# Kernel tuning notes

Hardware: AMD Instinct MI355X
Metric: run time of the kernel (lower is better)

## Reference

```python
import jax, jax.numpy as jnp
import numpy as np


def setup_inputs() -> dict:
    key = jax.random.key(0)
    k1, k2, k3, k4 = jax.random.split(key, 4)
    B, S, D = 16, 1024, 300      # batch, set_size, word_vector_dim
    K = 64                        # hidden_set_size == compressed_dim (element_dim)
    O = 256                       # set_representation_dim (output_dim)
    Xs = jax.random.normal(k1, (B, S, D), dtype=jnp.float32)
    # Linear(word_vector_dim -> hidden_set_size)
    W = jax.random.normal(k2, (K, D), dtype=jnp.float32) * (1.0 / np.sqrt(D))
    b = jax.random.normal(k3, (K,), dtype=jnp.float32) * 0.01
    # hidden_sets: (output_dim, hidden_set_size, element_dim) with xavier-normal scale
    xav = np.sqrt(2.0 / (K + K))
    hidden_sets = jax.random.normal(k4, (O, K, K), dtype=jnp.float32) * xav
    return {"Xs": Xs, "W": W, "b": b, "hidden_sets": hidden_sets}


def reference(Xs, W, b, hidden_sets):
    # compress: [B,S,D] @ [D,K] + b -> [B,S,K]
    Xc = jnp.einsum('bsd,kd->bsk', Xs, W) + b
    # bipartite_match: tensordot over element_dim -> [B,S,O,N] (N = hidden_set_size)
    G = jax.nn.relu(jnp.einsum('bsk,onk->bson', Xc, hidden_sets))
    # set_size (1024) > hidden_set_size (64): max over hidden-set axis, sum over set axis
    value = jnp.sum(jnp.max(G, axis=-1), axis=1)  # [B,O]
    return value
```

## Files before the change

kernel.cpp:

```cpp
#include <hip/hip_runtime.h>
#include <hip/hip_bf16.h>

#define B_  16
#define S_  1024
#define D_  300
#define DP  320
#define K_  64
#define O_  256
#define M_  (B_*S_)

#define LROW 80

typedef __attribute__((ext_vector_type(8)))  short s8b;
typedef __attribute__((ext_vector_type(4)))  float f32x4;
typedef __attribute__((ext_vector_type(16))) float f32x16;

#define MFMA16(a,b,c) __builtin_amdgcn_mfma_f32_16x16x32_bf16((a),(b),(c),0,0,0)
#define MFMA32(a,b,c) __builtin_amdgcn_mfma_f32_32x32x16_bf16((a),(b),(c),0,0,0)

__device__ __forceinline__ unsigned short bf16_bits(float f) {
    return __builtin_bit_cast(unsigned short, __float2bfloat16(f));
}

#define H_BLK  512
#define W_BLK  10
__global__ __launch_bounds__(256) void k_convert(
        const float* __restrict__ W, const float* __restrict__ H,
        __hip_bfloat16* __restrict__ Wb, __hip_bfloat16* __restrict__ Hb,
        float* __restrict__ out) {
    int bx = blockIdx.x, t = threadIdx.x;
    if (bx < H_BLK) {
        int g = (bx * 256 + t) * 8;
        float4 f0 = *(const float4*)(H + g);
        float4 f1 = *(const float4*)(H + g + 4);
        union { unsigned short us[8]; uint4 q; } pk;
        pk.us[0]=bf16_bits(f0.x); pk.us[1]=bf16_bits(f0.y);
        pk.us[2]=bf16_bits(f0.z); pk.us[3]=bf16_bits(f0.w);
        pk.us[4]=bf16_bits(f1.x); pk.us[5]=bf16_bits(f1.y);
        pk.us[6]=bf16_bits(f1.z); pk.us[7]=bf16_bits(f1.w);
        *(uint4*)(Hb + g) = pk.q;
        return;
    }
    if (bx == H_BLK + W_BLK) {
        float4 z = {0.f,0.f,0.f,0.f};
        float4* o4 = (float4*)out;
#pragma unroll
        for (int i = 0; i < 4; ++i) o4[t * 4 + i] = z;
        return;
    }
    int g = (bx - H_BLK) * 256 + t;
    int r = g / 40, c = (g - r * 40) * 8;
    const float* src = W + (size_t)r * D_;
    float v[8];
    if (c + 8 <= D_) {
        float4 f0 = *(const float4*)(src + c);
        float4 f1 = *(const float4*)(src + c + 4);
        v[0]=f0.x; v[1]=f0.y; v[2]=f0.z; v[3]=f0.w;
        v[4]=f1.x; v[5]=f1.y; v[6]=f1.z; v[7]=f1.w;
    } else {
#pragma unroll
        for (int j = 0; j < 8; ++j) v[j] = (c + j < D_) ? src[c + j] : 0.0f;
    }
    union { unsigned short us[8]; uint4 q; } pk;
#pragma unroll
    for (int j = 0; j < 8; ++j) pk.us[j] = bf16_bits(v[j]);
    *(uint4*)(Wb + (size_t)r * DP + c) = pk.q;
}

__global__ __launch_bounds__(256) void k_compress(
        const float* __restrict__ Xs,
        const __hip_bfloat16* __restrict__ Wb,
        const float* __restrict__ bias,
        __hip_bfloat16* __restrict__ Xc) {
    int tid  = threadIdx.x;
    int w    = tid >> 6, lane = tid & 63;
    int q    = lane >> 4, r = lane & 15;
    int row0 = blockIdx.x * 16;
    int col0 = w * 16;

    f32x4 acc0 = {0.f,0.f,0.f,0.f}, acc1 = {0.f,0.f,0.f,0.f};
    const float*          arow = Xs + (size_t)(row0 + r) * D_;
    const __hip_bfloat16* brow = Wb + (size_t)(col0 + r) * DP;
    const float4 z4 = {0.f,0.f,0.f,0.f};

#pragma unroll
    for (int ks = 0; ks < 10; ++ks) {
        int k0 = ks * 32 + q * 8;
        float4 f0 = (k0     < D_) ? *(const float4*)(arow + k0)     : z4;
        float4 f1 = (k0 + 4 < D_) ? *(const float4*)(arow + k0 + 4) : z4;
        union { unsigned short us[8]; s8b v; } pk;
        pk.us[0]=bf16_bits(f0.x); pk.us[1]=bf16_bits(f0.y);
        pk.us[2]=bf16_bits(f0.z); pk.us[3]=bf16_bits(f0.w);
        pk.us[4]=bf16_bits(f1.x); pk.us[5]=bf16_bits(f1.y);
        pk.us[6]=bf16_bits(f1.z); pk.us[7]=bf16_bits(f1.w);
        s8b b = __builtin_bit_cast(s8b, *(const uint4*)(brow + k0));
        if (ks & 1) acc1 = MFMA16(pk.v, b, acc1);
        else        acc0 = MFMA16(pk.v, b, acc0);
    }
#pragma unroll
    for (int i = 0; i < 4; ++i) {
        int orow = row0 + q * 4 + i;
        int c    = col0 + r;
        Xc[(size_t)orow * K_ + c] =
            __float2bfloat16(acc0[i] + acc1[i] + bias[c]);
    }
}

__global__ __launch_bounds__(256, 4) void k_fused(
        const __hip_bfloat16* __restrict__ Xc,
        const __hip_bfloat16* __restrict__ Hb,
        float* __restrict__ out) {
    __shared__ __hip_bfloat16 lx[2][64 * LROW];
    int tid   = threadIdx.x;
    int w     = tid >> 6, lane = tid & 63;
    int half  = lane >> 5, l31 = lane & 31;
    int bx    = blockIdx.x;
    int batch = bx >> 7;
    int oq    = (bx >> 1) & 63;
    int sh    = bx & 1;
    int o     = oq * 4 + w;

    s8b af[2][4];
#pragma unroll
    for (int nt = 0; nt < 2; ++nt) {
        const __hip_bfloat16* hrow =
            Hb + (size_t)(o * 64 + nt * 32 + l31) * 64 + half * 8;
#pragma unroll
        for (int ks = 0; ks < 4; ++ks)
            af[nt][ks] = __builtin_bit_cast(s8b, *(const uint4*)(hrow + ks * 16));
    }

    const __hip_bfloat16* xbase =
        Xc + ((size_t)batch * S_ + (size_t)sh * 512) * K_;

    int sr = tid >> 3, sc = tid & 7;

#pragma unroll
    for (int i = 0; i < 2; ++i) {
        int r = sr + i * 32;
        uint4 v = *(const uint4*)(xbase + (size_t)r * K_ + sc * 8);
        *(uint4*)(&lx[0][r * LROW + sc * 8]) = v;
    }
    __syncthreads();

    float total = 0.0f;
    for (int s = 0; s < 8; ++s) {
        uint4 npf[2];
        if (s < 7) {
            const __hip_bfloat16* nsrc = xbase + (size_t)(s + 1) * 64 * K_;
#pragma unroll
            for (int i = 0; i < 2; ++i)
                npf[i] = *(const uint4*)(nsrc + (size_t)(sr + i * 32) * K_ + sc * 8);
        }
        const __hip_bfloat16* buf = lx[s & 1];
#pragma unroll
        for (int t = 0; t < 2; ++t) {
            int rr = t * 32 + l31;
            s8b bf[4];
#pragma unroll
            for (int ks = 0; ks < 4; ++ks)
                bf[ks] = __builtin_bit_cast(s8b,
                    *(const uint4*)(&buf[rr * LROW + (2 * ks + half) * 8]));

            f32x16 a0 = {0.f,0.f,0.f,0.f,0.f,0.f,0.f,0.f,
                         0.f,0.f,0.f,0.f,0.f,0.f,0.f,0.f};
            f32x16 a1 = a0;
#pragma unroll
            for (int ks = 0; ks < 4; ++ks) {
                a0 = MFMA32(af[0][ks], bf[ks], a0);
                a1 = MFMA32(af[1][ks], bf[ks], a1);
            }
            float m0 = fmaxf(fmaxf(a0[0], a0[1]), a0[2]);
            m0 = fmaxf(fmaxf(m0, a0[3]), a0[4]);
            m0 = fmaxf(fmaxf(m0, a0[5]), a0[6]);
            m0 = fmaxf(m0, a0[7]);
            float m1 = fmaxf(fmaxf(a0[8], a0[9]), a0[10]);
            m1 = fmaxf(fmaxf(m1, a0[11]), a0[12]);
            m1 = fmaxf(fmaxf(m1, a0[13]), a0[14]);
            m1 = fmaxf(m1, a0[15]);
            float m2 = fmaxf(fmaxf(a1[0], a1[1]), a1[2]);
            m2 = fmaxf(fmaxf(m2, a1[3]), a1[4]);
            m2 = fmaxf(fmaxf(m2, a1[5]), a1[6]);
            m2 = fmaxf(m2, a1[7]);
            float m3 = fmaxf(fmaxf(a1[8], a1[9]), a1[10]);
            m3 = fmaxf(fmaxf(m3, a1[11]), a1[12]);
            m3 = fmaxf(fmaxf(m3, a1[13]), a1[14]);
            m3 = fmaxf(m3, a1[15]);
            float v = fmaxf(fmaxf(fmaxf(m0, m1), fmaxf(m2, m3)), 0.0f);
            v = fmaxf(v, __shfl_xor(v, 32));
            total += v;
        }
        if (s < 7) {
#pragma unroll
            for (int i = 0; i < 2; ++i) {
                int r = sr + i * 32;
                *(uint4*)(&lx[(s + 1) & 1][r * LROW + sc * 8]) = npf[i];
            }
            __syncthreads();
        }
    }
    total += __shfl_xor(total, 1);
    total += __shfl_xor(total, 2);
    total += __shfl_xor(total, 4);
    total += __shfl_xor(total, 8);
    total += __shfl_xor(total, 16);
    if (lane == 0) atomicAdd(out + batch * O_ + o, total);
}

extern "C" void kernel_launch(void* const* d_in, const int* in_sizes, int n_in,
                              void* d_out, int out_size, void* d_ws, size_t ws_size,
                              hipStream_t stream) {
    const float* Xs   = (const float*)d_in[0];
    const float* W    = (const float*)d_in[1];
    const float* bias = (const float*)d_in[2];
    const float* H    = (const float*)d_in[3];
    float* out = (float*)d_out;

    char* ws = (char*)d_ws;
    __hip_bfloat16* Wb = (__hip_bfloat16*)(ws);
    __hip_bfloat16* Hb = (__hip_bfloat16*)(ws + 40960);
    __hip_bfloat16* Xc = (__hip_bfloat16*)(ws + 2138112);

    k_convert <<<H_BLK + W_BLK + 1, 256, 0, stream>>>(W, H, Wb, Hb, out);
    k_compress<<<M_ / 16, 256, 0, stream>>>(Xs, Wb, bias, Xc);
    k_fused   <<<B_ * (O_ / 4) * 2, 256, 0, stream>>>(Xc, Hb, out);
}
```

Measured before the change: 107.9 us.

## Drop separate bf16 conversion kernel; convert W and H inline in consumers

Removes the k_convert launch and instead converts W to bf16 inside k_compress and H to bf16 inside k_fused while loading fragments; output zeroing moves to an extra block of k_compress. This saves one kernel launch and the round trip through workspace for converted weights, at the cost of redundant fp32 reads and conversions (each H slice is re-read by 32 blocks). Also wraps the MFMA loop in s_setprio to favour matrix issue.

```diff
diff --git a/kernel.cpp b/kernel.cpp
--- a/kernel.cpp
+++ b/kernel.cpp
@@ -4,7 +4,6 @@
 #define B_  16
 #define S_  1024
 #define D_  300
-#define DP  320
 #define K_  64
 #define O_  256
 #define M_  (B_*S_)
@@ -22,56 +21,28 @@
     return __builtin_bit_cast(unsigned short, __float2bfloat16(f));
 }
 
-#define H_BLK  512
-#define W_BLK  10
-__global__ __launch_bounds__(256) void k_convert(
-        const float* __restrict__ W, const float* __restrict__ H,
-        __hip_bfloat16* __restrict__ Wb, __hip_bfloat16* __restrict__ Hb,
-        float* __restrict__ out) {
-    int bx = blockIdx.x, t = threadIdx.x;
-    if (bx < H_BLK) {
-        int g = (bx * 256 + t) * 8;
-        float4 f0 = *(const float4*)(H + g);
-        float4 f1 = *(const float4*)(H + g + 4);
-        union { unsigned short us[8]; uint4 q; } pk;
-        pk.us[0]=bf16_bits(f0.x); pk.us[1]=bf16_bits(f0.y);
-        pk.us[2]=bf16_bits(f0.z); pk.us[3]=bf16_bits(f0.w);
-        pk.us[4]=bf16_bits(f1.x); pk.us[5]=bf16_bits(f1.y);
-        pk.us[6]=bf16_bits(f1.z); pk.us[7]=bf16_bits(f1.w);
-        *(uint4*)(Hb + g) = pk.q;
-        return;
-    }
-    if (bx == H_BLK + W_BLK) {
-        float4 z = {0.f,0.f,0.f,0.f};
-        float4* o4 = (float4*)out;
-#pragma unroll
-        for (int i = 0; i < 4; ++i) o4[t * 4 + i] = z;
-        return;
-    }
-    int g = (bx - H_BLK) * 256 + t;
-    int r = g / 40, c = (g - r * 40) * 8;
-    const float* src = W + (size_t)r * D_;
-    float v[8];
-    if (c + 8 <= D_) {
-        float4 f0 = *(const float4*)(src + c);
-        float4 f1 = *(const float4*)(src + c + 4);
-        v[0]=f0.x; v[1]=f0.y; v[2]=f0.z; v[3]=f0.w;
-        v[4]=f1.x; v[5]=f1.y; v[6]=f1.z; v[7]=f1.w;
-    } else {
-#pragma unroll
-        for (int j = 0; j < 8; ++j) v[j] = (c + j < D_) ? src[c + j] : 0.0f;
-    }
-    union { unsigned short us[8]; uint4 q; } pk;
-#pragma unroll
-    for (int j = 0; j < 8; ++j) pk.us[j] = bf16_bits(v[j]);
-    *(uint4*)(Wb + (size_t)r * DP + c) = pk.q;
+__device__ __forceinline__ s8b pack8(float4 f0, float4 f1) {
+    union { unsigned short us[8]; s8b v; } pk;
+    pk.us[0]=bf16_bits(f0.x); pk.us[1]=bf16_bits(f0.y);
+    pk.us[2]=bf16_bits(f0.z); pk.us[3]=bf16_bits(f0.w);
+    pk.us[4]=bf16_bits(f1.x); pk.us[5]=bf16_bits(f1.y);
+    pk.us[6]=bf16_bits(f1.z); pk.us[7]=bf16_bits(f1.w);
+    return pk.v;
 }
 
 __global__ __launch_bounds__(256) void k_compress(
         const float* __restrict__ Xs,
-        const __hip_bfloat16* __restrict__ Wb,
+        const float* __restrict__ W,
         const float* __restrict__ bias,
-        __hip_bfloat16* __restrict__ Xc) {
+        __hip_bfloat16* __restrict__ Xc,
+        float* __restrict__ out) {
+    if (blockIdx.x == M_ / 16) {
+        float4 z = {0.f,0.f,0.f,0.f};
+        float4* o4 = (float4*)out;
+#pragma unroll
+        for (int i = 0; i < 4; ++i) o4[threadIdx.x * 4 + i] = z;
+        return;
+    }
     int tid  = threadIdx.x;
     int w    = tid >> 6, lane = tid & 63;
     int q    = lane >> 4, r = lane & 15;
@@ -79,23 +50,21 @@
     int col0 = w * 16;
 
     f32x4 acc0 = {0.f,0.f,0.f,0.f}, acc1 = {0.f,0.f,0.f,0.f};
-    const float*          arow = Xs + (size_t)(row0 + r) * D_;
-    const __hip_bfloat16* brow = Wb + (size_t)(col0 + r) * DP;
+    const float* arow = Xs + (size_t)(row0 + r) * D_;
+    const float* brow = W  + (size_t)(col0 + r) * D_;
     const float4 z4 = {0.f,0.f,0.f,0.f};
 
 #pragma unroll
     for (int ks = 0; ks < 10; ++ks) {
         int k0 = ks * 32 + q * 8;
-        float4 f0 = (k0     < D_) ? *(const float4*)(arow + k0)     : z4;
-        float4 f1 = (k0 + 4 < D_) ? *(const float4*)(arow + k0 + 4) : z4;
-        union { unsigned short us[8]; s8b v; } pk;
-        pk.us[0]=bf16_bits(f0.x); pk.us[1]=bf16_bits(f0.y);
-        pk.us[2]=bf16_bits(f0.z); pk.us[3]=bf16_bits(f0.w);
-        pk.us[4]=bf16_bits(f1.x); pk.us[5]=bf16_bits(f1.y);
-        pk.us[6]=bf16_bits(f1.z); pk.us[7]=bf16_bits(f1.w);
-        s8b b = __builtin_bit_cast(s8b, *(const uint4*)(brow + k0));
-        if (ks & 1) acc1 = MFMA16(pk.v, b, acc1);
-        else        acc0 = MFMA16(pk.v, b, acc0);
+        float4 a0 = (k0     < D_) ? *(const float4*)(arow + k0)     : z4;
+        float4 a1 = (k0 + 4 < D_) ? *(const float4*)(arow + k0 + 4) : z4;
+        float4 b0 = (k0     < D_) ? *(const float4*)(brow + k0)     : z4;
+        float4 b1 = (k0 + 4 < D_) ? *(const float4*)(brow + k0 + 4) : z4;
+        s8b av = pack8(a0, a1);
+        s8b bv = pack8(b0, b1);
+        if (ks & 1) acc1 = MFMA16(av, bv, acc1);
+        else        acc0 = MFMA16(av, bv, acc0);
     }
 #pragma unroll
     for (int i = 0; i < 4; ++i) {
@@ -108,7 +77,7 @@
 
 __global__ __launch_bounds__(256, 4) void k_fused(
         const __hip_bfloat16* __restrict__ Xc,
-        const __hip_bfloat16* __restrict__ Hb,
+        const float* __restrict__ H,
         float* __restrict__ out) {
     __shared__ __hip_bfloat16 lx[2][64 * LROW];
     int tid   = threadIdx.x;
@@ -123,11 +92,14 @@
     s8b af[2][4];
 #pragma unroll
     for (int nt = 0; nt < 2; ++nt) {
-        const __hip_bfloat16* hrow =
-            Hb + (size_t)(o * 64 + nt * 32 + l31) * 64 + half * 8;
+        const float* hrow =
+            H + (size_t)(o * 64 + nt * 32 + l31) * 64 + half * 8;
 #pragma unroll
-        for (int ks = 0; ks < 4; ++ks)
-            af[nt][ks] = __builtin_bit_cast(s8b, *(const uint4*)(hrow + ks * 16));
+        for (int ks = 0; ks < 4; ++ks) {
+            float4 h0 = *(const float4*)(hrow + ks * 16);
+            float4 h1 = *(const float4*)(hrow + ks * 16 + 4);
+            af[nt][ks] = pack8(h0, h1);
+        }
     }
 
     const __hip_bfloat16* xbase =
@@ -165,11 +137,13 @@
             f32x16 a0 = {0.f,0.f,0.f,0.f,0.f,0.f,0.f,0.f,
                          0.f,0.f,0.f,0.f,0.f,0.f,0.f,0.f};
             f32x16 a1 = a0;
+            __builtin_amdgcn_s_setprio(1);
 #pragma unroll
             for (int ks = 0; ks < 4; ++ks) {
                 a0 = MFMA32(af[0][ks], bf[ks], a0);
                 a1 = MFMA32(af[1][ks], bf[ks], a1);
             }
+            __builtin_amdgcn_s_setprio(0);
             float m0 = fmaxf(fmaxf(a0[0], a0[1]), a0[2]);
             m0 = fmaxf(fmaxf(m0, a0[3]), a0[4]);
             m0 = fmaxf(fmaxf(m0, a0[5]), a0[6]);
@@ -216,12 +190,8 @@
     const float* H    = (const float*)d_in[3];
     float* out = (float*)d_out;
 
-    char* ws = (char*)d_ws;
-    __hip_bfloat16* Wb = (__hip_bfloat16*)(ws);
-    __hip_bfloat16* Hb = (__hip_bfloat16*)(ws + 40960);
-    __hip_bfloat16* Xc = (__hip_bfloat16*)(ws + 2138112);
+    __hip_bfloat16* Xc = (__hip_bfloat16*)d_ws;
 
-    k_convert <<<H_BLK + W_BLK + 1, 256, 0, stream>>>(W, H, Wb, Hb, out);
-    k_compress<<<M_ / 16, 256, 0, stream>>>(Xs, Wb, bias, Xc);
-    k_fused   <<<B_ * (O_ / 4) * 2, 256, 0, stream>>>(Xc, Hb, out);
+    k_compress<<<M_ / 16 + 1, 256, 0, stream>>>(Xs, W, bias, Xc, out);
+    k_fused   <<<B_ * (O_ / 4) * 2, 256, 0, stream>>>(Xc, H, out);
 }
```

Result: slower. 112.7 us (+4.5%).
